# Kernel tuning notes

Hardware: AMD Instinct MI355X
Metric: run time of the kernel (lower is better)

The kernel has to match this reference:

```python
import jax, jax.numpy as jnp
import numpy as np

N_NODES = 100000
DEG = 32
N_EDGES = N_NODES * DEG
N_FEAT = 128
N_CLASSES = 40
LN_EPS = 1e-5
CLAMP_MIN = 1e-5


def setup_inputs() -> dict:
    key = jax.random.key(0)
    k_h, k_lg, k_z, k_src, k_t1, k_t2 = jax.random.split(key, 6)
    h = jax.random.normal(k_h, (N_NODES, N_FEAT), dtype=jnp.float32)
    logits = jax.random.normal(k_lg, (N_NODES, N_CLASSES), dtype=jnp.float32)
    old_z = jax.random.uniform(k_z, (N_NODES,), dtype=jnp.float32)
    # uniform in-degree graph: every node receives exactly DEG messages
    dst = jnp.repeat(jnp.arange(N_NODES, dtype=jnp.int32), DEG)
    src = jax.random.randint(k_src, (N_EDGES,), 0, N_NODES, dtype=jnp.int32)
    in_degs = jnp.full((N_NODES,), float(DEG), dtype=jnp.float32)
    norm = 1.0 / in_degs  # GCN-style normalization constant per node
    tau_1 = jax.random.uniform(k_t1, (1,), dtype=jnp.float32)
    tau_2 = jax.random.uniform(k_t2, (1,), dtype=jnp.float32)
    return {"h": h, "logits": logits, "old_z": old_z, "norm": norm,
            "in_degs": in_degs, "tau_1": tau_1, "tau_2": tau_2,
            "src": src, "dst": dst}


def _node_layernorm(x):
    # LayerNorm over the node dimension, no affine (elementwise_affine=False)
    m = jnp.mean(x)
    v = jnp.var(x)
    return (x - m) * jax.lax.rsqrt(v + LN_EPS)


def reference(h, logits, old_z, norm, in_degs, tau_1, tau_2, src, dst):
    n = h.shape[0]
    c = logits.shape[1]
    # per-node predicted class, and per-edge neighbor prediction
    pred = jnp.argmax(logits, axis=1)            # [N]
    nbr_pred = pred[src]                          # [E]
    # f1: fraction of in-neighbors agreeing with the center node's prediction
    match = (nbr_pred == pred[dst]).astype(h.dtype)
    f1 = jax.ops.segment_sum(match, dst, num_segments=n) / in_degs
    # f2: entropy of the neighbor-prediction histogram per node
    counts = jnp.zeros((n, c), dtype=h.dtype).at[dst, nbr_pred].add(1.0)
    cnts_p = jnp.clip(counts / in_degs[:, None], CLAMP_MIN)
    f2 = -jnp.sum(cnts_p * jnp.log(cnts_p), axis=1)
    # both metrics are detached in the original
    f1 = jax.lax.stop_gradient(f1)
    f2 = jax.lax.stop_gradient(f2)
    norm_f1 = _node_layernorm(f1)
    norm_f2 = _node_layernorm(f2)
    # shared_tau=True path: uses externally provided tau_1 / tau_2
    z = jax.nn.sigmoid(-(norm_f1 - tau_1)) * jax.nn.sigmoid(-(norm_f2 - tau_2))
    gate = jnp.minimum(old_z, z)
    # sum aggregation of neighbor features, normalized and activated
    agg = jax.ops.segment_sum(h[src], dst, num_segments=n)   # [N, F]
    normagg = jax.nn.relu(agg * norm[:, None])
    new_h = h + gate[:, None] * normagg
    return new_h, z
```

## Files before the change

### kernel.cpp

```cpp
#include <hip/hip_runtime.h>
#include <math.h>

#define N_NODES 100000
#define DEG 32
#define N_FEAT 128
#define N_CLASSES 40

constexpr float LN_EPS = 1e-5f;
constexpr float E0 = 1.1512925465e-4f;

#define NODE_ITERS 8
#define NODES_PER_BLOCK 64
#define NB2 ((N_NODES + NODES_PER_BLOCK - 1) / NODES_PER_BLOCK)

#define NCHUNK 4
#define AGG_NPB 128
#define NBLK ((N_NODES + AGG_NPB - 1) / AGG_NPB)

typedef float    f4 __attribute__((ext_vector_type(4)));
typedef float    f2 __attribute__((ext_vector_type(2)));
typedef int      i4 __attribute__((ext_vector_type(4)));
typedef unsigned u2 __attribute__((ext_vector_type(2)));
typedef unsigned u4 __attribute__((ext_vector_type(4)));

__device__ __forceinline__ unsigned pk4_fp8(float a, float b, float c, float d) {
    int w = __builtin_amdgcn_cvt_pk_fp8_f32(a, b, 0, false);
    w = __builtin_amdgcn_cvt_pk_fp8_f32(c, d, w, true);
    return (unsigned)w;
}
__device__ __forceinline__ void accp8(float* a, u2 r) {
    f2 p;
    p = __builtin_amdgcn_cvt_pk_f32_fp8((int)r.x, false); a[0] += p.x; a[1] += p.y;
    p = __builtin_amdgcn_cvt_pk_f32_fp8((int)r.x, true);  a[2] += p.x; a[3] += p.y;
    p = __builtin_amdgcn_cvt_pk_f32_fp8((int)r.y, false); a[4] += p.x; a[5] += p.y;
    p = __builtin_amdgcn_cvt_pk_f32_fp8((int)r.y, true);  a[6] += p.x; a[7] += p.y;
}

__global__ void k_argmax(const float* __restrict__ logits,
                         const float* __restrict__ old_z,
                         const float* __restrict__ normv,
                         unsigned char* __restrict__ predb, f2* __restrict__ ozn) {
    int i = blockIdx.x * blockDim.x + threadIdx.x;
    if (i >= N_NODES) return;
    const float4* row = reinterpret_cast<const float4*>(logits + (size_t)i * N_CLASSES);
    float best = -INFINITY;
    int bidx = 0;
#pragma unroll
    for (int q = 0; q < N_CLASSES / 4; ++q) {
        float4 v = row[q];
        if (v.x > best) { best = v.x; bidx = 4 * q + 0; }
        if (v.y > best) { best = v.y; bidx = 4 * q + 1; }
        if (v.z > best) { best = v.z; bidx = 4 * q + 2; }
        if (v.w > best) { best = v.w; bidx = 4 * q + 3; }
    }
    predb[i] = (unsigned char)bidx;
    f2 oz; oz.x = old_z[i]; oz.y = normv[i];
    ozn[i] = oz;
}

__global__ void k_pack(const float* __restrict__ h, unsigned char* __restrict__ hb8) {
    int t = blockIdx.x * 256 + threadIdx.x;
    if (t >= N_NODES * 4) return;
    int node = t >> 2;
    int q    = t & 3;
    const f4* hp = (const f4*)(h + (size_t)node * N_FEAT + q * 32);
    f4 v0 = __builtin_nontemporal_load(hp + 0);
    f4 v1 = __builtin_nontemporal_load(hp + 1);
    f4 v2 = __builtin_nontemporal_load(hp + 2);
    f4 v3 = __builtin_nontemporal_load(hp + 3);
    f4 v4 = __builtin_nontemporal_load(hp + 4);
    f4 v5 = __builtin_nontemporal_load(hp + 5);
    f4 v6 = __builtin_nontemporal_load(hp + 6);
    f4 v7 = __builtin_nontemporal_load(hp + 7);
    u4 o0, o1;
    o0.x = pk4_fp8(v0.x, v0.y, v0.z, v0.w);
    o0.y = pk4_fp8(v1.x, v1.y, v1.z, v1.w);
    o0.z = pk4_fp8(v2.x, v2.y, v2.z, v2.w);
    o0.w = pk4_fp8(v3.x, v3.y, v3.z, v3.w);
    o1.x = pk4_fp8(v4.x, v4.y, v4.z, v4.w);
    o1.y = pk4_fp8(v5.x, v5.y, v5.z, v5.w);
    o1.z = pk4_fp8(v6.x, v6.y, v6.z, v6.w);
    o1.w = pk4_fp8(v7.x, v7.y, v7.z, v7.w);
    u4* op = (u4*)(hb8 + ((size_t)q * N_NODES + node) * 32);
    op[0] = o0;
    op[1] = o1;
}

__global__ void k_f1f2(const int* __restrict__ src,
                       const unsigned char* __restrict__ predb,
                       f2* __restrict__ f12, float* __restrict__ part) {
    const int tid  = threadIdx.x;
    const int lane = tid & 63;
    const int wave = tid >> 6;
    const int grp  = lane >> 5;
    const int j    = lane & 31;

    float acc_s1 = 0.f, acc_q1 = 0.f, acc_s2 = 0.f, acc_q2 = 0.f;

    for (int t = 0; t < NODE_ITERS; ++t) {
        int node = blockIdx.x * NODES_PER_BLOCK + t * 8 + wave * 2 + grp;
        if (node < N_NODES) {
            int s = src[node * DEG + j];
            int v = predb[s];
            int pv = predb[node];
            int c = 0;
#pragma unroll
            for (int k = 0; k < 32; ++k)
                c += (v == __shfl(v, k, 32)) ? 1 : 0;
            float cf = (float)c;
            float p  = cf * (1.0f / 32.0f);
            float ent  = (-p * logf(p)) / cf;
            float dstc = 1.0f / cf;
            float mt   = (v == pv) ? 1.0f : 0.0f;
#pragma unroll
            for (int off = 16; off >= 1; off >>= 1) {
                mt   += __shfl_xor(mt, off, 32);
                ent  += __shfl_xor(ent, off, 32);
                dstc += __shfl_xor(dstc, off, 32);
            }
            if (j == 0) {
                float f1v = mt * (1.0f / 32.0f);
                float f2v = ent + ((float)N_CLASSES - dstc) * E0;
                f2 o; o.x = f1v; o.y = f2v;
                f12[node] = o;
                acc_s1 += f1v; acc_q1 += f1v * f1v;
                acc_s2 += f2v; acc_q2 += f2v * f2v;
            }
        }
    }

#pragma unroll
    for (int off = 1; off < 64; off <<= 1) {
        acc_s1 += __shfl_xor(acc_s1, off);
        acc_q1 += __shfl_xor(acc_q1, off);
        acc_s2 += __shfl_xor(acc_s2, off);
        acc_q2 += __shfl_xor(acc_q2, off);
    }
    __shared__ float4 sred[4];
    if (lane == 0) sred[wave] = make_float4(acc_s1, acc_q1, acc_s2, acc_q2);
    __syncthreads();
    if (tid == 0) {
        float4 r = sred[0];
        for (int w = 1; w < 4; ++w) {
            float4 q = sred[w];
            r.x += q.x; r.y += q.y; r.z += q.z; r.w += q.w;
        }
        part[0 * NB2 + blockIdx.x] = r.x;
        part[1 * NB2 + blockIdx.x] = r.y;
        part[2 * NB2 + blockIdx.x] = r.z;
        part[3 * NB2 + blockIdx.x] = r.w;
    }
}

__global__ void k_scal(const float* __restrict__ part, float* __restrict__ scal,
                       int* __restrict__ ctr) {
    const int tid = threadIdx.x;
    if (tid < 16) ctr[tid] = 0;
    double s1 = 0, q1 = 0, s2 = 0, q2 = 0;
    for (int i = tid; i < NB2; i += 256) {
        s1 += (double)part[0 * NB2 + i];
        q1 += (double)part[1 * NB2 + i];
        s2 += (double)part[2 * NB2 + i];
        q2 += (double)part[3 * NB2 + i];
    }
    __shared__ double sd[256][4];
    sd[tid][0] = s1; sd[tid][1] = q1; sd[tid][2] = s2; sd[tid][3] = q2;
    __syncthreads();
    for (int st = 128; st > 0; st >>= 1) {
        if (tid < st) {
            sd[tid][0] += sd[tid + st][0];
            sd[tid][1] += sd[tid + st][1];
            sd[tid][2] += sd[tid + st][2];
            sd[tid][3] += sd[tid + st][3];
        }
        __syncthreads();
    }
    if (tid == 0) {
        double n = (double)N_NODES;
        double m1 = sd[0][0] / n, v1 = sd[0][1] / n - m1 * m1;
        double m2 = sd[0][2] / n, v2 = sd[0][3] / n - m2 * m2;
        scal[0] = (float)m1;
        scal[1] = (float)(1.0 / sqrt(v1 + (double)LN_EPS));
        scal[2] = (float)m2;
        scal[3] = (float)(1.0 / sqrt(v2 + (double)LN_EPS));
    }
}

__global__ __launch_bounds__(256) void k_aggc(
        const unsigned char* __restrict__ hb8, const float* __restrict__ h,
        const int* __restrict__ src, const f2* __restrict__ f12,
        const f2* __restrict__ ozn, const float* __restrict__ scal,
        const float* __restrict__ tau1, const float* __restrict__ tau2,
        int* __restrict__ ctr, float* __restrict__ out_h,
        float* __restrict__ out_z) {
    __shared__ int s_item;
    if (threadIdx.x == 0) {
        unsigned xcd;
        asm volatile("s_getreg_b32 %0, hwreg(HW_REG_XCC_ID)" : "=s"(xcd));
        xcd &= 3;
        int item = -1;
        for (int a = 0; a < NCHUNK; ++a) {
            int cc = (int)((xcd + a) & 3);
            int t = atomicAdd(&ctr[cc], 1);
            if (t < NBLK) { item = (cc << 16) | t; break; }
        }
        s_item = item;
    }
    __syncthreads();
    int item = s_item;
    if (item < 0) return;
    const int chunk = item >> 16;
    const int nb    = item & 0xffff;
    const int g = threadIdx.x >> 2;
    const int j = threadIdx.x & 3;

    const i4* src4 = (const i4*)src;
    const u2* base = (const u2*)(hb8 + (size_t)chunk * ((size_t)N_NODES * 32));

    const float m1 = scal[0], i1 = scal[1], m2 = scal[2], i2 = scal[3];
    const float t1 = tau1[0], t2 = tau2[0];

    for (int it = 0; it < 2; ++it) {
        const int node = nb * AGG_NPB + it * 64 + g;
        if (node >= N_NODES) continue;

        i4 sv0 = __builtin_nontemporal_load(&src4[node * 8 + j * 2]);
        i4 sv1 = __builtin_nontemporal_load(&src4[node * 8 + j * 2 + 1]);
        const f4* hp = (const f4*)(h + (size_t)node * N_FEAT + chunk * 32 + j * 8);
        f4 h0 = __builtin_nontemporal_load(hp);
        f4 h1 = __builtin_nontemporal_load(hp + 1);
        f2 fv = f12[node];
        f2 oz = ozn[node];

        float a[8];
#pragma unroll
        for (int q = 0; q < 8; ++q) a[q] = 0.f;

#pragma unroll
        for (int o = 0; o < 4; ++o) {
            int s0 = __shfl(sv0.x, o, 4);
            int s1 = __shfl(sv0.y, o, 4);
            int s2 = __shfl(sv0.z, o, 4);
            int s3 = __shfl(sv0.w, o, 4);
            int s4 = __shfl(sv1.x, o, 4);
            int s5 = __shfl(sv1.y, o, 4);
            int s6 = __shfl(sv1.z, o, 4);
            int s7 = __shfl(sv1.w, o, 4);
            u2 r0 = base[(size_t)s0 * 4 + j];
            u2 r1 = base[(size_t)s1 * 4 + j];
            u2 r2 = base[(size_t)s2 * 4 + j];
            u2 r3 = base[(size_t)s3 * 4 + j];
            u2 r4 = base[(size_t)s4 * 4 + j];
            u2 r5 = base[(size_t)s5 * 4 + j];
            u2 r6 = base[(size_t)s6 * 4 + j];
            u2 r7 = base[(size_t)s7 * 4 + j];
            accp8(a, r0); accp8(a, r1); accp8(a, r2); accp8(a, r3);
            accp8(a, r4); accp8(a, r5); accp8(a, r6); accp8(a, r7);
        }

        float nf1 = (fv.x - m1) * i1;
        float nf2 = (fv.y - m2) * i2;
        float z = (1.0f / (1.0f + expf(nf1 - t1))) *
                  (1.0f / (1.0f + expf(nf2 - t2)));
        float gg = fminf(oz.x, z) * oz.y;

        f4 o0, o1;
        o0.x = h0.x + gg * fmaxf(a[0], 0.f);
        o0.y = h0.y + gg * fmaxf(a[1], 0.f);
        o0.z = h0.z + gg * fmaxf(a[2], 0.f);
        o0.w = h0.w + gg * fmaxf(a[3], 0.f);
        o1.x = h1.x + gg * fmaxf(a[4], 0.f);
        o1.y = h1.y + gg * fmaxf(a[5], 0.f);
        o1.z = h1.z + gg * fmaxf(a[6], 0.f);
        o1.w = h1.w + gg * fmaxf(a[7], 0.f);
        f4* op = (f4*)(out_h + (size_t)node * N_FEAT + chunk * 32 + j * 8);
        __builtin_nontemporal_store(o0, op);
        __builtin_nontemporal_store(o1, op + 1);
        if (chunk == 0 && j == 0) out_z[node] = z;
    }
}

__global__ void k_agg(const float* __restrict__ h, const f2* __restrict__ ozn,
                      const int* __restrict__ src, const f2* __restrict__ f12,
                      const float* __restrict__ scal, const float* __restrict__ tau1,
                      const float* __restrict__ tau2,
                      float* __restrict__ out_h, float* __restrict__ out_z) {
    const int lane = threadIdx.x & 63;
    const int wave = threadIdx.x >> 6;
    const int grp  = lane >> 5;
    const int j    = lane & 31;
    const int node = blockIdx.x * 8 + wave * 2 + grp;
    if (node >= N_NODES) return;

    int sv = src[node * DEG + j];
    const float4* H4 = reinterpret_cast<const float4*>(h);
    float4 acc = make_float4(0.f, 0.f, 0.f, 0.f);
#pragma unroll
    for (int k = 0; k < DEG; ++k) {
        int s = __shfl(sv, k, 32);
        float4 r = H4[(size_t)s * (N_FEAT / 4) + j];
        acc.x += r.x; acc.y += r.y; acc.z += r.z; acc.w += r.w;
    }
    f2 fv = f12[node];
    f2 oz = ozn[node];
    float nf1 = (fv.x - scal[0]) * scal[1];
    float nf2 = (fv.y - scal[2]) * scal[3];
    float z = (1.0f / (1.0f + expf(nf1 - tau1[0]))) *
              (1.0f / (1.0f + expf(nf2 - tau2[0])));
    float gg = fminf(oz.x, z) * oz.y;
    float4 hrow = H4[(size_t)node * (N_FEAT / 4) + j];
    float4 o;
    o.x = hrow.x + gg * fmaxf(acc.x, 0.0f);
    o.y = hrow.y + gg * fmaxf(acc.y, 0.0f);
    o.z = hrow.z + gg * fmaxf(acc.z, 0.0f);
    o.w = hrow.w + gg * fmaxf(acc.w, 0.0f);
    reinterpret_cast<float4*>(out_h)[(size_t)node * (N_FEAT / 4) + j] = o;
    if (j == 0) out_z[node] = z;
}

extern "C" void kernel_launch(void* const* d_in, const int* in_sizes, int n_in,
                              void* d_out, int out_size, void* d_ws, size_t ws_size,
                              hipStream_t stream) {
    const float* h      = (const float*)d_in[0];
    const float* logits = (const float*)d_in[1];
    const float* old_z  = (const float*)d_in[2];
    const float* normv  = (const float*)d_in[3];
    const float* tau1   = (const float*)d_in[5];
    const float* tau2   = (const float*)d_in[6];
    const int*   src    = (const int*)d_in[7];

    float* out_h = (float*)d_out;
    float* out_z = out_h + (size_t)N_NODES * N_FEAT;

    float* w    = (float*)d_ws;
    f2*    f12  = (f2*)w;
    f2*    ozn  = f12 + N_NODES;
    float* part = (float*)(ozn + N_NODES);
    float* scal = part + 4 * NB2;
    int*   ctr  = (int*)(scal + 4);
    unsigned char* predb = (unsigned char*)(ctr + 16);
    size_t off_bytes = ((char*)(predb + N_NODES) - (char*)d_ws);
    off_bytes = (off_bytes + 255) & ~(size_t)255;
    unsigned char* hb8 = (unsigned char*)d_ws + off_bytes;
    size_t need = off_bytes + (size_t)N_NODES * N_FEAT;
    bool use_fp8 = (ws_size >= need);

    k_argmax<<<(N_NODES + 255) / 256, 256, 0, stream>>>(logits, old_z, normv,
                                                        predb, ozn);
    k_f1f2<<<NB2, 256, 0, stream>>>(src, predb, f12, part);
    k_scal<<<1, 256, 0, stream>>>(part, scal, ctr);
    if (use_fp8) {
        k_pack<<<(N_NODES * 4 + 255) / 256, 256, 0, stream>>>(h, hb8);
        k_aggc<<<NCHUNK * NBLK, 256, 0, stream>>>(hb8, h, src, f12, ozn, scal,
                                                  tau1, tau2, ctr, out_h, out_z);
    } else {
        k_agg<<<(N_NODES + 7) / 8, 256, 0, stream>>>(h, ozn, src, f12, scal,
                                                     tau1, tau2, out_h, out_z);
    }
}
```

Before: 190.5 us.

## Fuse argmax with fp8 packing and interleave two-node gathers in aggregation

The argmax and fp8 packing kernels become one prep kernel, with four threads per node sharing the argmax and merging by shuffle, which removes a launch and a pass. In the chunked aggregation kernel, the two nodes each thread handles are now gathered together instead of in sequence, giving more outstanding loads per thread. Index arithmetic for the gathers switches to 32-bit unsigned. In exchange, register pressure rises and the tie-break logic in the reduction is new.

```diff
diff --git a/kernel.cpp b/kernel.cpp
--- a/kernel.cpp
+++ b/kernel.cpp
@@ -36,54 +36,60 @@
     p = __builtin_amdgcn_cvt_pk_f32_fp8((int)r.y, true);  a[6] += p.x; a[7] += p.y;
 }
 
-__global__ void k_argmax(const float* __restrict__ logits,
-                         const float* __restrict__ old_z,
-                         const float* __restrict__ normv,
-                         unsigned char* __restrict__ predb, f2* __restrict__ ozn) {
-    int i = blockIdx.x * blockDim.x + threadIdx.x;
-    if (i >= N_NODES) return;
-    const float4* row = reinterpret_cast<const float4*>(logits + (size_t)i * N_CLASSES);
-    float best = -INFINITY;
-    int bidx = 0;
-#pragma unroll
-    for (int q = 0; q < N_CLASSES / 4; ++q) {
-        float4 v = row[q];
-        if (v.x > best) { best = v.x; bidx = 4 * q + 0; }
-        if (v.y > best) { best = v.y; bidx = 4 * q + 1; }
-        if (v.z > best) { best = v.z; bidx = 4 * q + 2; }
-        if (v.w > best) { best = v.w; bidx = 4 * q + 3; }
-    }
-    predb[i] = (unsigned char)bidx;
-    f2 oz; oz.x = old_z[i]; oz.y = normv[i];
-    ozn[i] = oz;
-}
-
-__global__ void k_pack(const float* __restrict__ h, unsigned char* __restrict__ hb8) {
+__global__ void k_prep(const float* __restrict__ logits, const float* __restrict__ h,
+                       const float* __restrict__ old_z, const float* __restrict__ normv,
+                       unsigned char* __restrict__ predb, f2* __restrict__ ozn,
+                       unsigned char* __restrict__ hb8, int do_pack) {
     int t = blockIdx.x * 256 + threadIdx.x;
     if (t >= N_NODES * 4) return;
     int node = t >> 2;
     int q    = t & 3;
-    const f4* hp = (const f4*)(h + (size_t)node * N_FEAT + q * 32);
-    f4 v0 = __builtin_nontemporal_load(hp + 0);
-    f4 v1 = __builtin_nontemporal_load(hp + 1);
-    f4 v2 = __builtin_nontemporal_load(hp + 2);
-    f4 v3 = __builtin_nontemporal_load(hp + 3);
-    f4 v4 = __builtin_nontemporal_load(hp + 4);
-    f4 v5 = __builtin_nontemporal_load(hp + 5);
-    f4 v6 = __builtin_nontemporal_load(hp + 6);
-    f4 v7 = __builtin_nontemporal_load(hp + 7);
-    u4 o0, o1;
-    o0.x = pk4_fp8(v0.x, v0.y, v0.z, v0.w);
-    o0.y = pk4_fp8(v1.x, v1.y, v1.z, v1.w);
-    o0.z = pk4_fp8(v2.x, v2.y, v2.z, v2.w);
-    o0.w = pk4_fp8(v3.x, v3.y, v3.z, v3.w);
-    o1.x = pk4_fp8(v4.x, v4.y, v4.z, v4.w);
-    o1.y = pk4_fp8(v5.x, v5.y, v5.z, v5.w);
-    o1.z = pk4_fp8(v6.x, v6.y, v6.z, v6.w);
-    o1.w = pk4_fp8(v7.x, v7.y, v7.z, v7.w);
-    u4* op = (u4*)(hb8 + ((size_t)q * N_NODES + node) * 32);
-    op[0] = o0;
-    op[1] = o1;
+
+    const f2* lp = (const f2*)(logits + (size_t)node * N_CLASSES + q * 10);
+    float best = -INFINITY;
+    int bidx = 0;
+#pragma unroll
+    for (int i = 0; i < 5; ++i) {
+        f2 v = lp[i];
+        int i0 = q * 10 + 2 * i;
+        if (v.x > best) { best = v.x; bidx = i0; }
+        if (v.y > best) { best = v.y; bidx = i0 + 1; }
+    }
+#pragma unroll
+    for (int off = 1; off < 4; off <<= 1) {
+        float ov = __shfl_xor(best, off, 4);
+        int   oi = __shfl_xor(bidx, off, 4);
+        if (ov > best || (ov == best && oi < bidx)) { best = ov; bidx = oi; }
+    }
+    if (q == 0) {
+        predb[node] = (unsigned char)bidx;
+        f2 oz; oz.x = old_z[node]; oz.y = normv[node];
+        ozn[node] = oz;
+    }
+
+    if (do_pack) {
+        const f4* hp = (const f4*)(h + (size_t)node * N_FEAT + q * 32);
+        f4 v0 = __builtin_nontemporal_load(hp + 0);
+        f4 v1 = __builtin_nontemporal_load(hp + 1);
+        f4 v2 = __builtin_nontemporal_load(hp + 2);
+        f4 v3 = __builtin_nontemporal_load(hp + 3);
+        f4 v4 = __builtin_nontemporal_load(hp + 4);
+        f4 v5 = __builtin_nontemporal_load(hp + 5);
+        f4 v6 = __builtin_nontemporal_load(hp + 6);
+        f4 v7 = __builtin_nontemporal_load(hp + 7);
+        u4 o0, o1;
+        o0.x = pk4_fp8(v0.x, v0.y, v0.z, v0.w);
+        o0.y = pk4_fp8(v1.x, v1.y, v1.z, v1.w);
+        o0.z = pk4_fp8(v2.x, v2.y, v2.z, v2.w);
+        o0.w = pk4_fp8(v3.x, v3.y, v3.z, v3.w);
+        o1.x = pk4_fp8(v4.x, v4.y, v4.z, v4.w);
+        o1.y = pk4_fp8(v5.x, v5.y, v5.z, v5.w);
+        o1.z = pk4_fp8(v6.x, v6.y, v6.z, v6.w);
+        o1.w = pk4_fp8(v7.x, v7.y, v7.z, v7.w);
+        u4* op = (u4*)(hb8 + ((size_t)q * N_NODES + node) * 32);
+        op[0] = o0;
+        op[1] = o1;
+    }
 }
 
 __global__ void k_f1f2(const int* __restrict__ src,
@@ -214,69 +220,107 @@
     const int g = threadIdx.x >> 2;
     const int j = threadIdx.x & 3;
 
+    const int nodeA = nb * AGG_NPB + g;
+    const int nodeB = nodeA + 64;
+    if (nodeA >= N_NODES) return;
+    const bool hasB = (nodeB < N_NODES);
+    const int nodeBc = hasB ? nodeB : nodeA;
+
     const i4* src4 = (const i4*)src;
     const u2* base = (const u2*)(hb8 + (size_t)chunk * ((size_t)N_NODES * 32));
 
     const float m1 = scal[0], i1 = scal[1], m2 = scal[2], i2 = scal[3];
     const float t1 = tau1[0], t2 = tau2[0];
 
-    for (int it = 0; it < 2; ++it) {
-        const int node = nb * AGG_NPB + it * 64 + g;
-        if (node >= N_NODES) continue;
-
-        i4 sv0 = __builtin_nontemporal_load(&src4[node * 8 + j * 2]);
-        i4 sv1 = __builtin_nontemporal_load(&src4[node * 8 + j * 2 + 1]);
-        const f4* hp = (const f4*)(h + (size_t)node * N_FEAT + chunk * 32 + j * 8);
-        f4 h0 = __builtin_nontemporal_load(hp);
-        f4 h1 = __builtin_nontemporal_load(hp + 1);
-        f2 fv = f12[node];
-        f2 oz = ozn[node];
-
-        float a[8];
-#pragma unroll
-        for (int q = 0; q < 8; ++q) a[q] = 0.f;
-
-#pragma unroll
-        for (int o = 0; o < 4; ++o) {
-            int s0 = __shfl(sv0.x, o, 4);
-            int s1 = __shfl(sv0.y, o, 4);
-            int s2 = __shfl(sv0.z, o, 4);
-            int s3 = __shfl(sv0.w, o, 4);
-            int s4 = __shfl(sv1.x, o, 4);
-            int s5 = __shfl(sv1.y, o, 4);
-            int s6 = __shfl(sv1.z, o, 4);
-            int s7 = __shfl(sv1.w, o, 4);
-            u2 r0 = base[(size_t)s0 * 4 + j];
-            u2 r1 = base[(size_t)s1 * 4 + j];
-            u2 r2 = base[(size_t)s2 * 4 + j];
-            u2 r3 = base[(size_t)s3 * 4 + j];
-            u2 r4 = base[(size_t)s4 * 4 + j];
-            u2 r5 = base[(size_t)s5 * 4 + j];
-            u2 r6 = base[(size_t)s6 * 4 + j];
-            u2 r7 = base[(size_t)s7 * 4 + j];
-            accp8(a, r0); accp8(a, r1); accp8(a, r2); accp8(a, r3);
-            accp8(a, r4); accp8(a, r5); accp8(a, r6); accp8(a, r7);
-        }
-
-        float nf1 = (fv.x - m1) * i1;
-        float nf2 = (fv.y - m2) * i2;
+    i4 svA0 = __builtin_nontemporal_load(&src4[nodeA * 8 + j * 2]);
+    i4 svA1 = __builtin_nontemporal_load(&src4[nodeA * 8 + j * 2 + 1]);
+    i4 svB0 = __builtin_nontemporal_load(&src4[nodeBc * 8 + j * 2]);
+    i4 svB1 = __builtin_nontemporal_load(&src4[nodeBc * 8 + j * 2 + 1]);
+
+    const f4* hpA = (const f4*)(h + (size_t)nodeA * N_FEAT + chunk * 32 + j * 8);
+    f4 hA0 = __builtin_nontemporal_load(hpA);
+    f4 hA1 = __builtin_nontemporal_load(hpA + 1);
+    const f4* hpB = (const f4*)(h + (size_t)nodeBc * N_FEAT + chunk * 32 + j * 8);
+    f4 hB0 = __builtin_nontemporal_load(hpB);
+    f4 hB1 = __builtin_nontemporal_load(hpB + 1);
+    f2 fvA = f12[nodeA], ozA = ozn[nodeA];
+    f2 fvB = f12[nodeBc], ozB = ozn[nodeBc];
+
+    float aA[8], aB[8];
+#pragma unroll
+    for (int q = 0; q < 8; ++q) { aA[q] = 0.f; aB[q] = 0.f; }
+
+#pragma unroll
+    for (int o = 0; o < 4; ++o) {
+        int a0 = __shfl(svA0.x, o, 4), a1 = __shfl(svA0.y, o, 4);
+        int a2 = __shfl(svA0.z, o, 4), a3 = __shfl(svA0.w, o, 4);
+        int a4 = __shfl(svA1.x, o, 4), a5 = __shfl(svA1.y, o, 4);
+        int a6 = __shfl(svA1.z, o, 4), a7 = __shfl(svA1.w, o, 4);
+        u2 rA0 = base[(unsigned)(a0 * 4 + j)];
+        u2 rA1 = base[(unsigned)(a1 * 4 + j)];
+        u2 rA2 = base[(unsigned)(a2 * 4 + j)];
+        u2 rA3 = base[(unsigned)(a3 * 4 + j)];
+        u2 rA4 = base[(unsigned)(a4 * 4 + j)];
+        u2 rA5 = base[(unsigned)(a5 * 4 + j)];
+        u2 rA6 = base[(unsigned)(a6 * 4 + j)];
+        u2 rA7 = base[(unsigned)(a7 * 4 + j)];
+        int b0 = __shfl(svB0.x, o, 4), b1 = __shfl(svB0.y, o, 4);
+        int b2 = __shfl(svB0.z, o, 4), b3 = __shfl(svB0.w, o, 4);
+        int b4 = __shfl(svB1.x, o, 4), b5 = __shfl(svB1.y, o, 4);
+        int b6 = __shfl(svB1.z, o, 4), b7 = __shfl(svB1.w, o, 4);
+        u2 rB0 = base[(unsigned)(b0 * 4 + j)];
+        u2 rB1 = base[(unsigned)(b1 * 4 + j)];
+        u2 rB2 = base[(unsigned)(b2 * 4 + j)];
+        u2 rB3 = base[(unsigned)(b3 * 4 + j)];
+        u2 rB4 = base[(unsigned)(b4 * 4 + j)];
+        u2 rB5 = base[(unsigned)(b5 * 4 + j)];
+        u2 rB6 = base[(unsigned)(b6 * 4 + j)];
+        u2 rB7 = base[(unsigned)(b7 * 4 + j)];
+        accp8(aA, rA0); accp8(aA, rA1); accp8(aA, rA2); accp8(aA, rA3);
+        accp8(aA, rA4); accp8(aA, rA5); accp8(aA, rA6); accp8(aA, rA7);
+        accp8(aB, rB0); accp8(aB, rB1); accp8(aB, rB2); accp8(aB, rB3);
+        accp8(aB, rB4); accp8(aB, rB5); accp8(aB, rB6); accp8(aB, rB7);
+    }
+
+    {
+        float nf1 = (fvA.x - m1) * i1;
+        float nf2 = (fvA.y - m2) * i2;
         float z = (1.0f / (1.0f + expf(nf1 - t1))) *
                   (1.0f / (1.0f + expf(nf2 - t2)));
-        float gg = fminf(oz.x, z) * oz.y;
-
+        float gg = fminf(ozA.x, z) * ozA.y;
         f4 o0, o1;
-        o0.x = h0.x + gg * fmaxf(a[0], 0.f);
-        o0.y = h0.y + gg * fmaxf(a[1], 0.f);
-        o0.z = h0.z + gg * fmaxf(a[2], 0.f);
-        o0.w = h0.w + gg * fmaxf(a[3], 0.f);
-        o1.x = h1.x + gg * fmaxf(a[4], 0.f);
-        o1.y = h1.y + gg * fmaxf(a[5], 0.f);
-        o1.z = h1.z + gg * fmaxf(a[6], 0.f);
-        o1.w = h1.w + gg * fmaxf(a[7], 0.f);
-        f4* op = (f4*)(out_h + (size_t)node * N_FEAT + chunk * 32 + j * 8);
+        o0.x = hA0.x + gg * fmaxf(aA[0], 0.f);
+        o0.y = hA0.y + gg * fmaxf(aA[1], 0.f);
+        o0.z = hA0.z + gg * fmaxf(aA[2], 0.f);
+        o0.w = hA0.w + gg * fmaxf(aA[3], 0.f);
+        o1.x = hA1.x + gg * fmaxf(aA[4], 0.f);
+        o1.y = hA1.y + gg * fmaxf(aA[5], 0.f);
+        o1.z = hA1.z + gg * fmaxf(aA[6], 0.f);
+        o1.w = hA1.w + gg * fmaxf(aA[7], 0.f);
+        f4* op = (f4*)(out_h + (size_t)nodeA * N_FEAT + chunk * 32 + j * 8);
         __builtin_nontemporal_store(o0, op);
         __builtin_nontemporal_store(o1, op + 1);
-        if (chunk == 0 && j == 0) out_z[node] = z;
+        if (chunk == 0 && j == 0) out_z[nodeA] = z;
+    }
+    if (hasB) {
+        float nf1 = (fvB.x - m1) * i1;
+        float nf2 = (fvB.y - m2) * i2;
+        float z = (1.0f / (1.0f + expf(nf1 - t1))) *
+                  (1.0f / (1.0f + expf(nf2 - t2)));
+        float gg = fminf(ozB.x, z) * ozB.y;
+        f4 o0, o1;
+        o0.x = hB0.x + gg * fmaxf(aB[0], 0.f);
+        o0.y = hB0.y + gg * fmaxf(aB[1], 0.f);
+        o0.z = hB0.z + gg * fmaxf(aB[2], 0.f);
+        o0.w = hB0.w + gg * fmaxf(aB[3], 0.f);
+        o1.x = hB1.x + gg * fmaxf(aB[4], 0.f);
+        o1.y = hB1.y + gg * fmaxf(aB[5], 0.f);
+        o1.z = hB1.z + gg * fmaxf(aB[6], 0.f);
+        o1.w = hB1.w + gg * fmaxf(aB[7], 0.f);
+        f4* op = (f4*)(out_h + (size_t)nodeB * N_FEAT + chunk * 32 + j * 8);
+        __builtin_nontemporal_store(o0, op);
+        __builtin_nontemporal_store(o1, op + 1);
+        if (chunk == 0 && j == 0) out_z[nodeB] = z;
     }
 }
 
@@ -345,12 +389,12 @@
     size_t need = off_bytes + (size_t)N_NODES * N_FEAT;
     bool use_fp8 = (ws_size >= need);
 
-    k_argmax<<<(N_NODES + 255) / 256, 256, 0, stream>>>(logits, old_z, normv,
-                                                        predb, ozn);
+    k_prep<<<(N_NODES * 4 + 255) / 256, 256, 0, stream>>>(logits, h, old_z, normv,
+                                                          predb, ozn, hb8,
+                                                          use_fp8 ? 1 : 0);
     k_f1f2<<<NB2, 256, 0, stream>>>(src, predb, f12, part);
     k_scal<<<1, 256, 0, stream>>>(part, scal, ctr);
     if (use_fp8) {
-        k_pack<<<(N_NODES * 4 + 255) / 256, 256, 0, stream>>>(h, hb8);
         k_aggc<<<NCHUNK * NBLK, 256, 0, stream>>>(hb8, h, src, f12, ozn, scal,
                                                   tau1, tau2, ctr, out_h, out_z);
     } else {
```

Result: faster. 175.2 us (-8.0%).
